# Kernel tuning notes

Hardware: AMD Instinct MI355X
Metric: run time of the kernel (lower is better)

## Reference

```python
import jax, jax.numpy as jnp
import numpy as np


def setup_inputs() -> dict:
    key = jax.random.key(0)
    k1, k2 = jax.random.split(key)
    x = jax.random.normal(k1, (16, 256, 128, 128), dtype=jnp.float32)
    # Conv2d(2, 1, 7, padding=3, bias=False) weight, OIHW layout
    conv_w = jax.random.normal(k2, (1, 2, 7, 7), dtype=jnp.float32) * 0.1
    return {"x": x, "conv_w": conv_w}


def reference(x, conv_w):
    # channel-wise mean and max pooling -> [B, 1, H, W] each
    avg_pool = jnp.mean(x, axis=1, keepdims=True)
    max_pool = jnp.max(x, axis=1, keepdims=True)
    cat = jnp.concatenate([avg_pool, max_pool], axis=1)  # [B, 2, H, W]
    # 7x7 conv, SAME padding (pad=3), NCHW / OIHW
    out = jax.lax.conv_general_dilated(
        cat, conv_w,
        window_strides=(1, 1),
        padding=((3, 3), (3, 3)),
        dimension_numbers=("NCHW", "OIHW", "NCHW"),
    )  # [B, 1, H, W]
    M = jax.nn.sigmoid(out)
    return x * M
```

## Files before the change

### kernel.cpp

```cpp
#include <hip/hip_runtime.h>
#include <math.h>

#define BB 16
#define CC 256
#define HH 128
#define WW 128
#define HWSZ (HH * WW)

typedef float floatx4 __attribute__((ext_vector_type(4)));

__global__ __launch_bounds__(256) void pool_kernel(const float* __restrict__ x,
                                                   float* __restrict__ avg_out,
                                                   float* __restrict__ max_out) {
    const int tf4   = threadIdx.x & 63;
    const int split = threadIdx.x >> 6;
    const int p0    = blockIdx.x * 256;
    const int b     = p0 >> 14;
    const int hw    = (p0 & (HWSZ - 1)) + tf4 * 4;

    const float* xb = x + (size_t)b * CC * HWSZ + hw;

    float4 s = make_float4(0.f, 0.f, 0.f, 0.f);
    float4 m = make_float4(-INFINITY, -INFINITY, -INFINITY, -INFINITY);

    const int c0 = split * 64;
    #pragma unroll 8
    for (int i = 0; i < 64; ++i) {
        float4 v = *(const float4*)(xb + (size_t)(c0 + i) * HWSZ);
        s.x += v.x; s.y += v.y; s.z += v.z; s.w += v.w;
        m.x = fmaxf(m.x, v.x); m.y = fmaxf(m.y, v.y);
        m.z = fmaxf(m.z, v.z); m.w = fmaxf(m.w, v.w);
    }

    __shared__ float4 sS[4][64];
    __shared__ float4 sM[4][64];
    sS[split][tf4] = s;
    sM[split][tf4] = m;
    __syncthreads();

    for (int off = 2; off >= 1; off >>= 1) {
        if (split < off) {
            float4 a  = sS[split][tf4], b2 = sS[split + off][tf4];
            a.x += b2.x; a.y += b2.y; a.z += b2.z; a.w += b2.w;
            sS[split][tf4] = a;
            float4 ma = sM[split][tf4], mb = sM[split + off][tf4];
            ma.x = fmaxf(ma.x, mb.x); ma.y = fmaxf(ma.y, mb.y);
            ma.z = fmaxf(ma.z, mb.z); ma.w = fmaxf(ma.w, mb.w);
            sM[split][tf4] = ma;
        }
        __syncthreads();
    }

    if (split == 0) {
        float4 a = sS[0][tf4];
        const float inv = 1.0f / CC;
        a.x *= inv; a.y *= inv; a.z *= inv; a.w *= inv;
        *(float4*)(avg_out + (size_t)b * HWSZ + hw) = a;
        *(float4*)(max_out + (size_t)b * HWSZ + hw) = sM[0][tf4];
    }
}

__global__ __launch_bounds__(256) void convmul_kernel(const float* __restrict__ x,
                                                      const float* __restrict__ avg_p,
                                                      const float* __restrict__ max_p,
                                                      const float* __restrict__ wgt,
                                                      float* __restrict__ out) {
    __shared__ float sw[98];
    __shared__ float sMl[256];

    const int tid = threadIdx.x;
    if (tid < 98) sw[tid] = wgt[tid];
    __syncthreads();

    const int bid   = blockIdx.x;
    const int hc    = bid & 1;
    const int strip = bid >> 1;
    const int b     = strip >> 6;
    const int h0    = (strip & 63) * 2;

    {
        const int hl = tid >> 7;
        const int w  = tid & 127;
        const int h  = h0 + hl;
        const float* ap = avg_p + (size_t)b * HWSZ;
        const float* mp = max_p + (size_t)b * HWSZ;

        float acc = 0.f;
        #pragma unroll
        for (int kh = 0; kh < 7; ++kh) {
            const int hh = h + kh - 3;
            if (hh < 0 || hh >= HH) continue;
            #pragma unroll
            for (int kw = 0; kw < 7; ++kw) {
                const int ww2 = w + kw - 3;
                if (ww2 < 0 || ww2 >= WW) continue;
                const int off = hh * WW + ww2;
                acc += ap[off] * sw[kh * 7 + kw];
                acc += mp[off] * sw[49 + kh * 7 + kw];
            }
        }
        sMl[tid] = 1.0f / (1.0f + expf(-acc));
    }
    __syncthreads();

    const int g    = tid & 63;
    const int csub = tid >> 6;
    const floatx4 mv = ((const floatx4*)sMl)[g];

    const size_t base = (size_t)b * CC * HWSZ
                      + (size_t)(hc * 128 + csub) * HWSZ
                      + (size_t)h0 * WW + (size_t)g * 4;
    const float* xp = x + base;
    float*       op = out + base;

    #pragma unroll 8
    for (int c = 0; c < 32; ++c) {
        const size_t coff = (size_t)c * 4 * HWSZ;
        floatx4 xv = __builtin_nontemporal_load((const floatx4*)(xp + coff));
        __builtin_nontemporal_store(xv * mv, (floatx4*)(op + coff));
    }
}

extern "C" void kernel_launch(void* const* d_in, const int* in_sizes, int n_in,
                              void* d_out, int out_size, void* d_ws, size_t ws_size,
                              hipStream_t stream) {
    const float* x   = (const float*)d_in[0];
    const float* wgt = (const float*)d_in[1];
    float* out = (float*)d_out;

    float* avg_p = (float*)d_ws;
    float* max_p = avg_p + (size_t)BB * HWSZ;

    pool_kernel<<<1024, 256, 0, stream>>>(x, avg_p, max_p);
    convmul_kernel<<<2048, 256, 0, stream>>>(x, avg_p, max_p, wgt, out);
}
```

Baseline: 145.5 us.

## Process batch in quarter chunks so the multiply pass rereads x from cache

Splits the pool and conv-multiply kernels into four launches each over groups of four batches. Each group's slice of x can then stay in the large last-level cache between the pooling read and the scaling read. Nontemporal loads and stores are replaced with normal ones so the data is retained in cache. The pool kernel also moves to 8 channel splits of 32. The cost is more kernel launches and smaller grids per launch.

Measured after the change: 189.8 us. +30.4%, slower.

```diff
diff --git a/kernel.cpp b/kernel.cpp
--- a/kernel.cpp
+++ b/kernel.cpp
@@ -9,36 +9,36 @@
 
 typedef float floatx4 __attribute__((ext_vector_type(4)));
 
-__global__ __launch_bounds__(256) void pool_kernel(const float* __restrict__ x,
-                                                   float* __restrict__ avg_out,
-                                                   float* __restrict__ max_out) {
-    const int tf4   = threadIdx.x & 63;
-    const int split = threadIdx.x >> 6;
-    const int p0    = blockIdx.x * 256;
-    const int b     = p0 >> 14;
-    const int hw    = (p0 & (HWSZ - 1)) + tf4 * 4;
+__global__ __launch_bounds__(256) void pool_q_kernel(const float* __restrict__ x,
+                                                     float* __restrict__ avg_out,
+                                                     float* __restrict__ max_out,
+                                                     int b0) {
+    const int tf4   = threadIdx.x & 31;
+    const int split = threadIdx.x >> 5;
+    const int tile  = blockIdx.x;
+    const int b     = b0 + (tile >> 7);
+    const int hw    = (tile & 127) * 128 + tf4 * 4;
 
-    const float* xb = x + (size_t)b * CC * HWSZ + hw;
+    const float* xb = x + (size_t)(b * CC + split * 32) * HWSZ + hw;
 
     float4 s = make_float4(0.f, 0.f, 0.f, 0.f);
     float4 m = make_float4(-INFINITY, -INFINITY, -INFINITY, -INFINITY);
 
-    const int c0 = split * 64;
     #pragma unroll 8
-    for (int i = 0; i < 64; ++i) {
-        float4 v = *(const float4*)(xb + (size_t)(c0 + i) * HWSZ);
+    for (int i = 0; i < 32; ++i) {
+        float4 v = *(const float4*)(xb + (size_t)i * HWSZ);
         s.x += v.x; s.y += v.y; s.z += v.z; s.w += v.w;
         m.x = fmaxf(m.x, v.x); m.y = fmaxf(m.y, v.y);
         m.z = fmaxf(m.z, v.z); m.w = fmaxf(m.w, v.w);
     }
 
-    __shared__ float4 sS[4][64];
-    __shared__ float4 sM[4][64];
+    __shared__ float4 sS[8][32];
+    __shared__ float4 sM[8][32];
     sS[split][tf4] = s;
     sM[split][tf4] = m;
     __syncthreads();
 
-    for (int off = 2; off >= 1; off >>= 1) {
+    for (int off = 4; off >= 1; off >>= 1) {
         if (split < off) {
             float4 a  = sS[split][tf4], b2 = sS[split + off][tf4];
             a.x += b2.x; a.y += b2.y; a.z += b2.z; a.w += b2.w;
@@ -60,11 +60,12 @@
     }
 }
 
-__global__ __launch_bounds__(256) void convmul_kernel(const float* __restrict__ x,
-                                                      const float* __restrict__ avg_p,
-                                                      const float* __restrict__ max_p,
-                                                      const float* __restrict__ wgt,
-                                                      float* __restrict__ out) {
+__global__ __launch_bounds__(256) void convmul_q_kernel(const float* __restrict__ x,
+                                                        const float* __restrict__ avg_p,
+                                                        const float* __restrict__ max_p,
+                                                        const float* __restrict__ wgt,
+                                                        float* __restrict__ out,
+                                                        int b0) {
     __shared__ float sw[98];
     __shared__ float sMl[256];
 
@@ -75,7 +76,7 @@
     const int bid   = blockIdx.x;
     const int hc    = bid & 1;
     const int strip = bid >> 1;
-    const int b     = strip >> 6;
+    const int b     = b0 + (strip >> 6);
     const int h0    = (strip & 63) * 2;
 
     {
@@ -116,8 +117,8 @@
     #pragma unroll 8
     for (int c = 0; c < 32; ++c) {
         const size_t coff = (size_t)c * 4 * HWSZ;
-        floatx4 xv = __builtin_nontemporal_load((const floatx4*)(xp + coff));
-        __builtin_nontemporal_store(xv * mv, (floatx4*)(op + coff));
+        floatx4 xv = *(const floatx4*)(xp + coff);
+        *(floatx4*)(op + coff) = xv * mv;
     }
 }
 
@@ -131,6 +132,8 @@
     float* avg_p = (float*)d_ws;
     float* max_p = avg_p + (size_t)BB * HWSZ;
 
-    pool_kernel<<<1024, 256, 0, stream>>>(x, avg_p, max_p);
-    convmul_kernel<<<2048, 256, 0, stream>>>(x, avg_p, max_p, wgt, out);
+    for (int q = 0; q < 4; ++q) {
+        pool_q_kernel<<<512, 256, 0, stream>>>(x, avg_p, max_p, q * 4);
+        convmul_q_kernel<<<512, 256, 0, stream>>>(x, avg_p, max_p, wgt, out, q * 4);
+    }
 }
```
